# Optimization experiments

Hardware: AMD Instinct MI355X
Metric: run time of the kernel (lower is better)

The kernel has to match this reference:

```python
import jax, jax.numpy as jnp
import numpy as np

D_MODEL = 1024
N_HEADS = 16
HEAD_DIM = D_MODEL // N_HEADS


def setup_inputs() -> dict:
    key = jax.random.key(0)
    ks = jax.random.split(key, 12)
    B, S = 1, 4096
    s = 1.0 / np.sqrt(D_MODEL)
    return {
        "query": jax.random.normal(ks[0], (B, S, D_MODEL), jnp.float32),
        "key": jax.random.normal(ks[1], (B, S, D_MODEL), jnp.float32),
        "value": jax.random.normal(ks[2], (B, S, D_MODEL), jnp.float32),
        "attention_mask": jnp.ones((B, S), jnp.int32),
        "Wq": jax.random.normal(ks[3], (D_MODEL, D_MODEL), jnp.float32) * s,
        "bq": jax.random.normal(ks[4], (D_MODEL,), jnp.float32) * s,
        "Wk": jax.random.normal(ks[5], (D_MODEL, D_MODEL), jnp.float32) * s,
        "bk": jax.random.normal(ks[6], (D_MODEL,), jnp.float32) * s,
        "Wv": jax.random.normal(ks[7], (D_MODEL, D_MODEL), jnp.float32) * s,
        "bv": jax.random.normal(ks[8], (D_MODEL,), jnp.float32) * s,
        "Wo": jax.random.normal(ks[9], (D_MODEL, D_MODEL), jnp.float32) * s,
        "bo": jax.random.normal(ks[10], (D_MODEL,), jnp.float32) * s,
    }


def reference(query, key, value, attention_mask, Wq, bq, Wk, bk, Wv, bv, Wo, bo):
    B = query.shape[0]

    def split_heads(x):  # [B,S,D] -> [B,H,S,Dh]
        return x.reshape(B, -1, N_HEADS, HEAD_DIM).transpose(0, 2, 1, 3)

    q = split_heads(query @ Wq + bq)
    k = split_heads(key @ Wk + bk)
    v = split_heads(value @ Wv + bv)

    scores = jnp.einsum("bhqd,bhkd->bhqk", q, k) / np.sqrt(HEAD_DIM)
    # 2D mask [B, Skv] -> [B,1,1,Skv]; 0 positions filled with -1e9
    mask = attention_mask[:, None, None, :]
    scores = jnp.where(mask == 0, jnp.float32(-1e9), scores)
    weights = jax.nn.softmax(scores, axis=-1)
    out = jnp.einsum("bhqk,bhkd->bhqd", weights, v)
    out = out.transpose(0, 2, 1, 3).reshape(B, -1, D_MODEL)
    return out @ Wo + bo
```

## Files before the change

### kernel.cpp

```cpp
#include <hip/hip_runtime.h>
#include <hip/hip_bf16.h>
#include <cstdint>

typedef __attribute__((ext_vector_type(8))) short short8;
typedef __attribute__((ext_vector_type(4))) float floatx4;
typedef unsigned short u16;

#define D_MODEL 1024
#define S_LEN 4096
#define N_HEADS 16
#define HEAD_DIM 64
#define SCALE_LOG2E 0.18033688f

__device__ __forceinline__ u16 f2bf(float x) {
    union { float f; uint32_t u; } v; v.f = x;
    uint32_t u = v.u;
    u += 0x7fffu + ((u >> 16) & 1u);
    return (u16)(u >> 16);
}

__device__ __forceinline__ void load_lds16(const u16* g, u16* l) {
    __builtin_amdgcn_global_load_lds(
        (const __attribute__((address_space(1))) uint32_t*)g,
        (__attribute__((address_space(3))) uint32_t*)l, 16, 0, 0);
}

struct Conv3 { const float* s[3]; u16* d[3]; };
__global__ __launch_bounds__(256) void convert3(Conv3 a, int n4) {
    const int z = blockIdx.y;
    const float* __restrict__ src = a.s[z];
    u16* __restrict__ dst = a.d[z];
    int i = blockIdx.x * 256 + threadIdx.x;
    if (i >= n4) return;
    float4 v = reinterpret_cast<const float4*>(src)[i];
    ushort4 o;
    o.x = f2bf(v.x); o.y = f2bf(v.y); o.z = f2bf(v.z); o.w = f2bf(v.w);
    reinterpret_cast<ushort4*>(dst)[i] = o;
}

__global__ __launch_bounds__(64) void mask_prep(const int* __restrict__ m,
                                                float* __restrict__ madd,
                                                int* __restrict__ clean) {
    const int t = blockIdx.x, lane = threadIdx.x;
    const int v = m[t * 64 + lane];
    madd[t * 64 + lane] = (v == 0) ? -1.0e30f : 0.f;
    const unsigned long long bal = __ballot(v != 0);
    if (lane == 0) clean[t] = (bal == ~0ull) ? 1 : 0;
}

struct Tr4 { const float* s[4]; u16* d[4]; float scale[4]; };
__global__ __launch_bounds__(256) void transpose4(Tr4 a, int R, int C) {
    __shared__ u16 tile[32][34];
    const int z = blockIdx.z;
    const float* __restrict__ in = a.s[z];
    u16* __restrict__ out = a.d[z];
    const float sc = a.scale[z];
    const int tx = threadIdx.x, ty = threadIdx.y;
    const int c0 = blockIdx.x * 32, r0 = blockIdx.y * 32;
    #pragma unroll
    for (int j = 0; j < 32; j += 8)
        tile[ty + j][tx] = f2bf(in[(size_t)(r0 + ty + j) * C + c0 + tx] * sc);
    __syncthreads();
    #pragma unroll
    for (int j = 0; j < 32; j += 8)
        out[(size_t)(c0 + ty + j) * R + r0 + tx] = tile[tx][ty + j];
}

template <typename OutT>
__device__ __forceinline__ void gemm_bt_core(const u16* __restrict__ A, const u16* __restrict__ Bt,
                                             const float* __restrict__ bias, OutT* __restrict__ C,
                                             int M, int N, int K, int bx, int by, int trC,
                                             float bscale) {
    __shared__ u16 As[128 * 64];
    __shared__ u16 Bs[128 * 64];
    const int tid = threadIdx.x;
    const int wave = tid >> 6, lane = tid & 63;
    const int quad = lane >> 4, n16 = lane & 15;
    const int wm = wave >> 1, wn = wave & 1;
    const int m0 = by * 128, n0 = bx * 128;
    const int rl = lane >> 3, cl = lane & 7;

    floatx4 acc[4][4];
    #pragma unroll
    for (int i = 0; i < 4; ++i)
        #pragma unroll
        for (int t = 0; t < 4; ++t) acc[i][t] = (floatx4)0.f;

    for (int kt = 0; kt < K; kt += 64) {
        __syncthreads();
        #pragma unroll
        for (int u = 0; u < 4; ++u) {
            const int r = wave * 32 + u * 8 + rl;
            const int c = cl ^ (rl & 7);
            load_lds16(&A[(size_t)(m0 + r) * K + kt + c * 8], &As[(wave * 32 + u * 8) * 64]);
            load_lds16(&Bt[(size_t)(n0 + r) * K + kt + c * 8], &Bs[(wave * 32 + u * 8) * 64]);
        }
        __syncthreads();
        #pragma unroll
        for (int kk = 0; kk < 2; ++kk) {
            short8 a[4], b[4];
            #pragma unroll
            for (int i = 0; i < 4; ++i) {
                const int sw = ((kk * 4 + quad) ^ (n16 & 7)) * 8;
                a[i] = *reinterpret_cast<const short8*>(&As[(wm * 64 + i * 16 + n16) * 64 + sw]);
            }
            #pragma unroll
            for (int t = 0; t < 4; ++t) {
                const int sw = ((kk * 4 + quad) ^ (n16 & 7)) * 8;
                b[t] = *reinterpret_cast<const short8*>(&Bs[(wn * 64 + t * 16 + n16) * 64 + sw]);
            }
            #pragma unroll
            for (int i = 0; i < 4; ++i)
                #pragma unroll
                for (int t = 0; t < 4; ++t)
                    acc[i][t] = __builtin_amdgcn_mfma_f32_16x16x32_bf16(a[i], b[t], acc[i][t], 0, 0, 0);
        }
    }
    #pragma unroll
    for (int t = 0; t < 4; ++t) {
        const int col = n0 + wn * 64 + t * 16 + n16;
        const float bvs = bias[col] * bscale;
        #pragma unroll
        for (int i = 0; i < 4; ++i) {
            #pragma unroll
            for (int r = 0; r < 4; ++r) {
                const int row = m0 + wm * 64 + i * 16 + quad * 4 + r;
                const float val = acc[i][t][r] + bvs;
                const size_t idx = trC ? ((size_t)col * M + row) : ((size_t)row * N + col);
                if constexpr (sizeof(OutT) == 2) C[idx] = f2bf(val);
                else                             C[idx] = val;
            }
        }
    }
}

struct QkvArgs {
    const u16* A[3]; const u16* B[3]; const float* bias[3]; u16* C[3]; float bscale[3];
};

__global__ __launch_bounds__(256) void gemm_qkv(QkvArgs args, int M, int N, int K) {
    const int z = blockIdx.z;
    gemm_bt_core<u16>(args.A[z], args.B[z], args.bias[z], args.C[z], M, N, K,
                      blockIdx.x, blockIdx.y, z == 2 ? 1 : 0, args.bscale[z]);
}

__global__ __launch_bounds__(256) void gemm_out(const u16* __restrict__ A, const u16* __restrict__ Bt,
                                                const float* __restrict__ bias, float* __restrict__ C,
                                                int M, int N, int K) {
    gemm_bt_core<float>(A, Bt, bias, C, M, N, K, blockIdx.x, blockIdx.y, 0, 1.0f);
}

__global__ __launch_bounds__(512) void flash_attn(const u16* __restrict__ Q, const u16* __restrict__ Kb,
                                                  const u16* __restrict__ Vt,
                                                  const float* __restrict__ madd,
                                                  const int* __restrict__ clean,
                                                  u16* __restrict__ O) {
    __shared__ u16 Ks[3 * 64 * 64];
    __shared__ u16 Vs[3 * 64 * 64];
    __shared__ u16 Ps[8][16 * 64];
    const int tid = threadIdx.x;
    const int wave = tid >> 6, lane = tid & 63;
    const int quad = lane >> 4, n16 = lane & 15;
    const int bid = blockIdx.x;
    const int h = (bid & 7) * 2 + ((bid >> 3) & 1);
    const int qt = bid >> 4;
    const int hd = h * HEAD_DIM;
    const int q0 = qt * 128 + wave * 16;

    const int rl = lane >> 3, cl = lane & 7;
    const int swz = n16 & 7;
    const int stg_row = wave * 8 + rl;
    const int stg_c = (cl ^ (rl & 7)) * 8;
    const int ldst = (wave * 8) * 64;

    short8 b_q[2];
    #pragma unroll
    for (int kk = 0; kk < 2; ++kk)
        b_q[kk] = *reinterpret_cast<const short8*>(
            &Q[(size_t)(q0 + n16) * D_MODEL + hd + kk * 32 + quad * 8]);

    short8 vone;
    #pragma unroll
    for (int i = 0; i < 8; ++i) vone[i] = (short)0x3F80;

    floatx4 o_acc[4];
    floatx4 l_acc = (floatx4)0.f;
    #pragma unroll
    for (int t = 0; t < 4; ++t) o_acc[t] = (floatx4)0.f;

    #pragma unroll
    for (int p = 0; p < 2; ++p) {
        load_lds16(&Kb[(size_t)(p * 64 + stg_row) * D_MODEL + hd + stg_c], &Ks[p * 4096 + ldst]);
        load_lds16(&Vt[(size_t)(hd + stg_row) * S_LEN + p * 64 + stg_c], &Vs[p * 4096 + ldst]);
    }

    int cur = 0;
    #pragma unroll 1
    for (int it = 0; it < 64; ++it) {
        asm volatile("s_waitcnt vmcnt(2)\n\ts_barrier" ::: "memory");

        const int nb = (cur >= 1) ? cur - 1 : 2;
        const int kn = ((it + 2) & 63) * 64;
        load_lds16(&Kb[(size_t)(kn + stg_row) * D_MODEL + hd + stg_c], &Ks[nb * 4096 + ldst]);
        load_lds16(&Vt[(size_t)(hd + stg_row) * S_LEN + kn + stg_c], &Vs[nb * 4096 + ldst]);

        const u16* KsC = &Ks[cur * 4096];
        const u16* VsC = &Vs[cur * 4096];

        floatx4 s[4];
        #pragma unroll
        for (int t = 0; t < 4; ++t) {
            s[t] = (floatx4)0.f;
            #pragma unroll
            for (int kk = 0; kk < 2; ++kk) {
                const int sw = ((kk * 4 + quad) ^ swz) * 8;
                short8 ak = *reinterpret_cast<const short8*>(&KsC[(t * 16 + n16) * 64 + sw]);
                s[t] = __builtin_amdgcn_mfma_f32_16x16x32_bf16(ak, b_q[kk], s[t], 0, 0, 0);
            }
        }
        if (clean[it]) {
            #pragma unroll
            for (int t = 0; t < 4; ++t) {
                const float p0 = __builtin_amdgcn_exp2f(s[t][0]);
                const float p1 = __builtin_amdgcn_exp2f(s[t][1]);
                const float p2 = __builtin_amdgcn_exp2f(s[t][2]);
                const float p3 = __builtin_amdgcn_exp2f(s[t][3]);
                union { __hip_bfloat162 h; uint32_t u; } pa, pb;
                pa.h = __float22bfloat162_rn(make_float2(p0, p1));
                pb.h = __float22bfloat162_rn(make_float2(p2, p3));
                uint2 w; w.x = pa.u; w.y = pb.u;
                const int cw = t * 2 + (quad >> 1);
                *reinterpret_cast<uint2*>(
                    &Ps[wave][n16 * 64 + ((cw ^ swz) * 8 + (quad & 1) * 4)]) = w;
            }
        } else {
            const int k0 = it * 64;
            #pragma unroll
            for (int t = 0; t < 4; ++t) {
                const float4 mv = *reinterpret_cast<const float4*>(&madd[k0 + t * 16 + quad * 4]);
                const float p0 = __builtin_amdgcn_exp2f(s[t][0] + mv.x);
                const float p1 = __builtin_amdgcn_exp2f(s[t][1] + mv.y);
                const float p2 = __builtin_amdgcn_exp2f(s[t][2] + mv.z);
                const float p3 = __builtin_amdgcn_exp2f(s[t][3] + mv.w);
                union { __hip_bfloat162 h; uint32_t u; } pa, pb;
                pa.h = __float22bfloat162_rn(make_float2(p0, p1));
                pb.h = __float22bfloat162_rn(make_float2(p2, p3));
                uint2 w; w.x = pa.u; w.y = pb.u;
                const int cw = t * 2 + (quad >> 1);
                *reinterpret_cast<uint2*>(
                    &Ps[wave][n16 * 64 + ((cw ^ swz) * 8 + (quad & 1) * 4)]) = w;
            }
        }
        asm volatile("s_waitcnt lgkmcnt(0)" ::: "memory");
        short8 ap[2];
        #pragma unroll
        for (int kkv = 0; kkv < 2; ++kkv)
            ap[kkv] = *reinterpret_cast<const short8*>(
                &Ps[wave][n16 * 64 + ((kkv * 4 + quad) ^ swz) * 8]);
        asm volatile("" ::: "memory");
        #pragma unroll
        for (int kkv = 0; kkv < 2; ++kkv) {
            l_acc = __builtin_amdgcn_mfma_f32_16x16x32_bf16(ap[kkv], vone, l_acc, 0, 0, 0);
            #pragma unroll
            for (int t = 0; t < 4; ++t) {
                const int sw = ((kkv * 4 + quad) ^ swz) * 8;
                short8 bv = *reinterpret_cast<const short8*>(&VsC[(t * 16 + n16) * 64 + sw]);
                o_acc[t] = __builtin_amdgcn_mfma_f32_16x16x32_bf16(ap[kkv], bv, o_acc[t], 0, 0, 0);
            }
        }
        cur = (cur >= 2) ? 0 : cur + 1;
    }
    asm volatile("s_waitcnt vmcnt(0)" ::: "memory");
    float lir[4];
    #pragma unroll
    for (int r = 0; r < 4; ++r) lir[r] = 1.f / l_acc[r];
    #pragma unroll
    for (int t = 0; t < 4; ++t)
        #pragma unroll
        for (int r = 0; r < 4; ++r)
            O[(size_t)(q0 + quad * 4 + r) * D_MODEL + hd + t * 16 + n16] =
                f2bf(o_acc[t][r] * lir[r]);
}

extern "C" void kernel_launch(void* const* d_in, const int* in_sizes, int n_in,
                              void* d_out, int out_size, void* d_ws, size_t ws_size,
                              hipStream_t stream) {
    const float* query = (const float*)d_in[0];
    const float* key   = (const float*)d_in[1];
    const float* value = (const float*)d_in[2];
    const int*   mask  = (const int*)d_in[3];
    const float* Wq = (const float*)d_in[4];
    const float* bq = (const float*)d_in[5];
    const float* Wk = (const float*)d_in[6];
    const float* bk = (const float*)d_in[7];
    const float* Wv = (const float*)d_in[8];
    const float* bv = (const float*)d_in[9];
    const float* Wo = (const float*)d_in[10];
    const float* bo = (const float*)d_in[11];
    float* out = (float*)d_out;

    char* ws = (char*)d_ws;
    const size_t SZ_SD = (size_t)S_LEN * D_MODEL * 2;
    const size_t SZ_W  = (size_t)D_MODEL * D_MODEL * 2;
    u16* qb  = (u16*)(ws);
    u16* kb  = (u16*)(ws + SZ_SD);
    u16* vb  = (u16*)(ws + 2 * SZ_SD);
    u16* Wqt = (u16*)(ws + 3 * SZ_SD);
    u16* Wkt = (u16*)(ws + 3 * SZ_SD + SZ_W);
    u16* Wvt = (u16*)(ws + 3 * SZ_SD + 2 * SZ_W);
    u16* Wot = (u16*)(ws + 3 * SZ_SD + 3 * SZ_W);
    u16* Qp  = (u16*)(ws + 3 * SZ_SD + 4 * SZ_W);
    u16* Kp  = (u16*)(ws + 4 * SZ_SD + 4 * SZ_W);
    u16* Vpt = (u16*)(ws + 5 * SZ_SD + 4 * SZ_W);
    float* maddf = (float*)(ws + 6 * SZ_SD + 4 * SZ_W);
    int* cleanf  = (int*)(ws + 6 * SZ_SD + 4 * SZ_W + S_LEN * sizeof(float));
    u16* Oa  = kb;

    const int n4 = S_LEN * D_MODEL / 4;
    Conv3 cv;
    cv.s[0] = query; cv.s[1] = key; cv.s[2] = value;
    cv.d[0] = qb;    cv.d[1] = kb;  cv.d[2] = vb;
    convert3<<<dim3(n4 / 256, 3), 256, 0, stream>>>(cv, n4);

    mask_prep<<<dim3(S_LEN / 64), 64, 0, stream>>>(mask, maddf, cleanf);

    Tr4 tr;
    tr.s[0] = Wq; tr.s[1] = Wk; tr.s[2] = Wv; tr.s[3] = Wo;
    tr.d[0] = Wqt; tr.d[1] = Wkt; tr.d[2] = Wvt; tr.d[3] = Wot;
    tr.scale[0] = SCALE_LOG2E; tr.scale[1] = 1.f; tr.scale[2] = 1.f; tr.scale[3] = 1.f;
    transpose4<<<dim3(32, 32, 4), dim3(32, 8), 0, stream>>>(tr, D_MODEL, D_MODEL);

    QkvArgs qa;
    qa.A[0] = qb;  qa.A[1] = kb;  qa.A[2] = vb;
    qa.B[0] = Wqt; qa.B[1] = Wkt; qa.B[2] = Wvt;
    qa.bias[0] = bq; qa.bias[1] = bk; qa.bias[2] = bv;
    qa.C[0] = Qp; qa.C[1] = Kp; qa.C[2] = Vpt;
    qa.bscale[0] = SCALE_LOG2E; qa.bscale[1] = 1.f; qa.bscale[2] = 1.f;
    gemm_qkv<<<dim3(8, 32, 3), 256, 0, stream>>>(qa, S_LEN, D_MODEL, D_MODEL);

    flash_attn<<<dim3(512), 512, 0, stream>>>(Qp, Kp, Vpt, maddf, cleanf, Oa);

    gemm_out<<<dim3(8, 32), 256, 0, stream>>>(Oa, Wot, bo, out, S_LEN, D_MODEL, D_MODEL);
}
```

Before: 286.6 us.

## Triple-buffer GEMM LDS staging and merge preprocessing kernels into one launch

The GEMM core now uses three LDS buffers and issues global-to-LDS loads two K-tiles ahead, with a single vmcnt wait plus barrier per iteration instead of two syncthreads. This aims to overlap memory latency with MFMA work. The transposed V store is vectorized to ushort4 writes. The convert, transpose and mask kernels are fused into one launch to cut launch overhead. In exchange, LDS use triples to 96KB per block, which lowers occupancy, and the tail iterations issue redundant wrapped-around prefetches.

```diff
diff --git a/kernel.cpp b/kernel.cpp
--- a/kernel.cpp
+++ b/kernel.cpp
@@ -25,45 +25,48 @@
         (__attribute__((address_space(3))) uint32_t*)l, 16, 0, 0);
 }
 
-struct Conv3 { const float* s[3]; u16* d[3]; };
-__global__ __launch_bounds__(256) void convert3(Conv3 a, int n4) {
-    const int z = blockIdx.y;
-    const float* __restrict__ src = a.s[z];
-    u16* __restrict__ dst = a.d[z];
-    int i = blockIdx.x * 256 + threadIdx.x;
-    if (i >= n4) return;
-    float4 v = reinterpret_cast<const float4*>(src)[i];
-    ushort4 o;
-    o.x = f2bf(v.x); o.y = f2bf(v.y); o.z = f2bf(v.z); o.w = f2bf(v.w);
-    reinterpret_cast<ushort4*>(dst)[i] = o;
-}
-
-__global__ __launch_bounds__(64) void mask_prep(const int* __restrict__ m,
-                                                float* __restrict__ madd,
-                                                int* __restrict__ clean) {
-    const int t = blockIdx.x, lane = threadIdx.x;
-    const int v = m[t * 64 + lane];
-    madd[t * 64 + lane] = (v == 0) ? -1.0e30f : 0.f;
-    const unsigned long long bal = __ballot(v != 0);
-    if (lane == 0) clean[t] = (bal == ~0ull) ? 1 : 0;
-}
-
-struct Tr4 { const float* s[4]; u16* d[4]; float scale[4]; };
-__global__ __launch_bounds__(256) void transpose4(Tr4 a, int R, int C) {
+#define PREP_CONV 12288
+#define PREP_TR   4096
+struct PrepArgs {
+    const float* cs[3]; u16* cd[3];
+    const float* ts[4]; u16* td[4]; float tscale[4];
+    const int* mask; float* madd; int* clean;
+};
+__global__ __launch_bounds__(256) void prep(PrepArgs a) {
     __shared__ u16 tile[32][34];
-    const int z = blockIdx.z;
-    const float* __restrict__ in = a.s[z];
-    u16* __restrict__ out = a.d[z];
-    const float sc = a.scale[z];
-    const int tx = threadIdx.x, ty = threadIdx.y;
-    const int c0 = blockIdx.x * 32, r0 = blockIdx.y * 32;
-    #pragma unroll
-    for (int j = 0; j < 32; j += 8)
-        tile[ty + j][tx] = f2bf(in[(size_t)(r0 + ty + j) * C + c0 + tx] * sc);
-    __syncthreads();
-    #pragma unroll
-    for (int j = 0; j < 32; j += 8)
-        out[(size_t)(c0 + ty + j) * R + r0 + tx] = tile[tx][ty + j];
+    const int bx = blockIdx.x;
+    const int tid = threadIdx.x;
+    if (bx < PREP_CONV) {
+        const int z = bx >> 12;
+        const int i = (bx & 4095) * 256 + tid;
+        float4 v = reinterpret_cast<const float4*>(a.cs[z])[i];
+        ushort4 o;
+        o.x = f2bf(v.x); o.y = f2bf(v.y); o.z = f2bf(v.z); o.w = f2bf(v.w);
+        reinterpret_cast<ushort4*>(a.cd[z])[i] = o;
+    } else if (bx < PREP_CONV + PREP_TR) {
+        const int b = bx - PREP_CONV;
+        const int z = b >> 10;
+        const int t = b & 1023;
+        const float* __restrict__ in = a.ts[z];
+        u16* __restrict__ out = a.td[z];
+        const float sc = a.tscale[z];
+        const int c0 = (t & 31) * 32, r0 = (t >> 5) * 32;
+        const int tx = tid & 31, ty = tid >> 5;
+        #pragma unroll
+        for (int j = 0; j < 32; j += 8)
+            tile[ty + j][tx] = f2bf(in[(size_t)(r0 + ty + j) * D_MODEL + c0 + tx] * sc);
+        __syncthreads();
+        #pragma unroll
+        for (int j = 0; j < 32; j += 8)
+            out[(size_t)(c0 + ty + j) * D_MODEL + r0 + tx] = tile[tx][ty + j];
+    } else {
+        const int b = bx - PREP_CONV - PREP_TR;
+        const int i = b * 256 + tid;
+        const int v = a.mask[i];
+        a.madd[i] = (v == 0) ? -1.0e30f : 0.f;
+        const unsigned long long bal = __ballot(v != 0);
+        if ((tid & 63) == 0) a.clean[b * 4 + (tid >> 6)] = (bal == ~0ull) ? 1 : 0;
+    }
 }
 
 template <typename OutT>
@@ -71,14 +74,17 @@
                                              const float* __restrict__ bias, OutT* __restrict__ C,
                                              int M, int N, int K, int bx, int by, int trC,
                                              float bscale) {
-    __shared__ u16 As[128 * 64];
-    __shared__ u16 Bs[128 * 64];
+    __shared__ u16 As[3][128 * 64];
+    __shared__ u16 Bs[3][128 * 64];
     const int tid = threadIdx.x;
     const int wave = tid >> 6, lane = tid & 63;
     const int quad = lane >> 4, n16 = lane & 15;
     const int wm = wave >> 1, wn = wave & 1;
     const int m0 = by * 128, n0 = bx * 128;
     const int rl = lane >> 3, cl = lane & 7;
+    const int stg_c = (cl ^ (rl & 7)) * 8;
+    const int swz = n16 & 7;
+    const int KI = K >> 6;
 
     floatx4 acc[4][4];
     #pragma unroll
@@ -86,49 +92,80 @@
         #pragma unroll
         for (int t = 0; t < 4; ++t) acc[i][t] = (floatx4)0.f;
 
-    for (int kt = 0; kt < K; kt += 64) {
-        __syncthreads();
+    #pragma unroll
+    for (int p = 0; p < 2; ++p) {
         #pragma unroll
         for (int u = 0; u < 4; ++u) {
             const int r = wave * 32 + u * 8 + rl;
-            const int c = cl ^ (rl & 7);
-            load_lds16(&A[(size_t)(m0 + r) * K + kt + c * 8], &As[(wave * 32 + u * 8) * 64]);
-            load_lds16(&Bt[(size_t)(n0 + r) * K + kt + c * 8], &Bs[(wave * 32 + u * 8) * 64]);
-        }
-        __syncthreads();
+            load_lds16(&A[(size_t)(m0 + r) * K + p * 64 + stg_c], &As[p][(wave * 32 + u * 8) * 64]);
+            load_lds16(&Bt[(size_t)(n0 + r) * K + p * 64 + stg_c], &Bs[p][(wave * 32 + u * 8) * 64]);
+        }
+    }
+
+    int cur = 0;
+    #pragma unroll 1
+    for (int it = 0; it < KI; ++it) {
+        asm volatile("s_waitcnt vmcnt(8)\n\ts_barrier" ::: "memory");
+        const int nb = (cur >= 1) ? cur - 1 : 2;
+        const int kn = ((it + 2) & (KI - 1)) * 64;
+        #pragma unroll
+        for (int u = 0; u < 4; ++u) {
+            const int r = wave * 32 + u * 8 + rl;
+            load_lds16(&A[(size_t)(m0 + r) * K + kn + stg_c], &As[nb][(wave * 32 + u * 8) * 64]);
+            load_lds16(&Bt[(size_t)(n0 + r) * K + kn + stg_c], &Bs[nb][(wave * 32 + u * 8) * 64]);
+        }
         #pragma unroll
         for (int kk = 0; kk < 2; ++kk) {
+            const int sw = ((kk * 4 + quad) ^ swz) * 8;
             short8 a[4], b[4];
             #pragma unroll
-            for (int i = 0; i < 4; ++i) {
-                const int sw = ((kk * 4 + quad) ^ (n16 & 7)) * 8;
-                a[i] = *reinterpret_cast<const short8*>(&As[(wm * 64 + i * 16 + n16) * 64 + sw]);
-            }
-            #pragma unroll
-            for (int t = 0; t < 4; ++t) {
-                const int sw = ((kk * 4 + quad) ^ (n16 & 7)) * 8;
-                b[t] = *reinterpret_cast<const short8*>(&Bs[(wn * 64 + t * 16 + n16) * 64 + sw]);
-            }
+            for (int i = 0; i < 4; ++i)
+                a[i] = *reinterpret_cast<const short8*>(&As[cur][(wm * 64 + i * 16 + n16) * 64 + sw]);
+            #pragma unroll
+            for (int t = 0; t < 4; ++t)
+                b[t] = *reinterpret_cast<const short8*>(&Bs[cur][(wn * 64 + t * 16 + n16) * 64 + sw]);
             #pragma unroll
             for (int i = 0; i < 4; ++i)
                 #pragma unroll
                 for (int t = 0; t < 4; ++t)
                     acc[i][t] = __builtin_amdgcn_mfma_f32_16x16x32_bf16(a[i], b[t], acc[i][t], 0, 0, 0);
         }
-    }
-    #pragma unroll
-    for (int t = 0; t < 4; ++t) {
-        const int col = n0 + wn * 64 + t * 16 + n16;
-        const float bvs = bias[col] * bscale;
-        #pragma unroll
-        for (int i = 0; i < 4; ++i) {
-            #pragma unroll
-            for (int r = 0; r < 4; ++r) {
-                const int row = m0 + wm * 64 + i * 16 + quad * 4 + r;
-                const float val = acc[i][t][r] + bvs;
-                const size_t idx = trC ? ((size_t)col * M + row) : ((size_t)row * N + col);
-                if constexpr (sizeof(OutT) == 2) C[idx] = f2bf(val);
-                else                             C[idx] = val;
+        cur = (cur >= 2) ? 0 : cur + 1;
+    }
+    asm volatile("s_waitcnt vmcnt(0)" ::: "memory");
+
+    if (trC) {
+        if constexpr (sizeof(OutT) == 2) {
+            #pragma unroll
+            for (int t = 0; t < 4; ++t) {
+                const int col = n0 + wn * 64 + t * 16 + n16;
+                const float bvs = bias[col] * bscale;
+                #pragma unroll
+                for (int i = 0; i < 4; ++i) {
+                    const int row = m0 + wm * 64 + i * 16 + quad * 4;
+                    ushort4 o;
+                    o.x = f2bf(acc[i][t][0] + bvs);
+                    o.y = f2bf(acc[i][t][1] + bvs);
+                    o.z = f2bf(acc[i][t][2] + bvs);
+                    o.w = f2bf(acc[i][t][3] + bvs);
+                    *reinterpret_cast<ushort4*>(&C[(size_t)col * M + row]) = o;
+                }
+            }
+        }
+    } else {
+        #pragma unroll
+        for (int t = 0; t < 4; ++t) {
+            const int col = n0 + wn * 64 + t * 16 + n16;
+            const float bvs = bias[col] * bscale;
+            #pragma unroll
+            for (int i = 0; i < 4; ++i) {
+                #pragma unroll
+                for (int r = 0; r < 4; ++r) {
+                    const int row = m0 + wm * 64 + i * 16 + quad * 4 + r;
+                    const float val = acc[i][t][r] + bvs;
+                    if constexpr (sizeof(OutT) == 2) C[(size_t)row * N + col] = f2bf(val);
+                    else                             C[(size_t)row * N + col] = val;
+                }
             }
         }
     }
@@ -316,19 +353,14 @@
     int* cleanf  = (int*)(ws + 6 * SZ_SD + 4 * SZ_W + S_LEN * sizeof(float));
     u16* Oa  = kb;
 
-    const int n4 = S_LEN * D_MODEL / 4;
-    Conv3 cv;
-    cv.s[0] = query; cv.s[1] = key; cv.s[2] = value;
-    cv.d[0] = qb;    cv.d[1] = kb;  cv.d[2] = vb;
-    convert3<<<dim3(n4 / 256, 3), 256, 0, stream>>>(cv, n4);
-
-    mask_prep<<<dim3(S_LEN / 64), 64, 0, stream>>>(mask, maddf, cleanf);
-
-    Tr4 tr;
-    tr.s[0] = Wq; tr.s[1] = Wk; tr.s[2] = Wv; tr.s[3] = Wo;
-    tr.d[0] = Wqt; tr.d[1] = Wkt; tr.d[2] = Wvt; tr.d[3] = Wot;
-    tr.scale[0] = SCALE_LOG2E; tr.scale[1] = 1.f; tr.scale[2] = 1.f; tr.scale[3] = 1.f;
-    transpose4<<<dim3(32, 32, 4), dim3(32, 8), 0, stream>>>(tr, D_MODEL, D_MODEL);
+    PrepArgs pa;
+    pa.cs[0] = query; pa.cs[1] = key; pa.cs[2] = value;
+    pa.cd[0] = qb;    pa.cd[1] = kb;  pa.cd[2] = vb;
+    pa.ts[0] = Wq; pa.ts[1] = Wk; pa.ts[2] = Wv; pa.ts[3] = Wo;
+    pa.td[0] = Wqt; pa.td[1] = Wkt; pa.td[2] = Wvt; pa.td[3] = Wot;
+    pa.tscale[0] = SCALE_LOG2E; pa.tscale[1] = 1.f; pa.tscale[2] = 1.f; pa.tscale[3] = 1.f;
+    pa.mask = mask; pa.madd = maddf; pa.clean = cleanf;
+    prep<<<dim3(PREP_CONV + PREP_TR + 16), 256, 0, stream>>>(pa);
 
     QkvArgs qa;
     qa.A[0] = qb;  qa.A[1] = kb;  qa.A[2] = vb;
```

Result: slower. 294.2 us (+2.7%).
